# Kernel tuning notes

Measured on AMD Instinct MI355X. Metric: run time of the kernel, lower is better.

The kernel has to match this reference:

```python
import jax, jax.numpy as jnp
import numpy as np

NUM_STREAMS = 4
DIM = 256
SINKHORN_ITERS = 10
SINKHORN_TAU = 0.05


def sinkhorn_log(logits, num_iters=SINKHORN_ITERS, tau=SINKHORN_TAU):
    n = logits.shape[-1]
    z = logits / tau
    log_marginal = -jnp.log(jnp.asarray(float(n), dtype=logits.dtype))

    def body(carry, _):
        u, v = carry
        u = log_marginal - jax.scipy.special.logsumexp(z + v[None, :], axis=1)
        v = log_marginal - jax.scipy.special.logsumexp(z + u[:, None], axis=0)
        return (u, v), None

    u0 = jnp.zeros((n,), dtype=z.dtype)
    v0 = jnp.zeros((n,), dtype=z.dtype)
    (u, v), _ = jax.lax.scan(body, (u0, v0), None, length=num_iters)
    return jnp.exp(z + u[:, None] + v[None, :]) * n


def setup_inputs() -> dict:
    key = jax.random.key(0)
    k_res, k_w = jax.random.split(key)
    B = 65536
    residuals = jax.random.normal(k_res, (B, NUM_STREAMS, DIM), dtype=jnp.float32)
    # h_res_logits: -8 everywhere, 0 on diagonal (as in __init__)
    h_res_logits = jnp.full((NUM_STREAMS, NUM_STREAMS), -8.0, dtype=jnp.float32)
    h_res_logits = h_res_logits.at[jnp.arange(NUM_STREAMS), jnp.arange(NUM_STREAMS)].set(0.0)
    # h_pre_logits: -8 everywhere, 0 at init_residual_index=0
    h_pre_logits = jnp.full((NUM_STREAMS,), -8.0, dtype=jnp.float32).at[0].set(0.0)
    h_post_logits = jnp.zeros((NUM_STREAMS,), dtype=jnp.float32)
    # branch Linear(dim, dim, bias=False): weight (out, in), y = x @ W.T
    bound = 1.0 / np.sqrt(DIM)
    W_branch = jax.random.uniform(k_w, (DIM, DIM), dtype=jnp.float32, minval=-bound, maxval=bound)
    return {
        "residuals": residuals,
        "h_res_logits": h_res_logits,
        "h_pre_logits": h_pre_logits,
        "h_post_logits": h_post_logits,
        "W_branch": W_branch,
    }


def reference(residuals, h_res_logits, h_pre_logits, h_post_logits, W_branch):
    # residuals: (B, S, D)
    h_res = sinkhorn_log(h_res_logits)                     # (S, S) doubly-stochastic * n
    h_pre = jax.nn.softmax(h_pre_logits)                   # (S,)
    h_post = jax.nn.softmax(h_post_logits)                 # (S,)
    residuals_mixed = jnp.einsum('st,bsd->btd', h_res, residuals)
    branch_input = jnp.einsum('s,bsd->bd', h_pre, residuals)
    branch_output = branch_input @ W_branch.T              # (B, D)
    depth_out = jnp.einsum('bd,s->bsd', branch_output, h_post)
    return residuals_mixed + depth_out
```

## Files before the change

### kernel.cpp

```cpp
#include <hip/hip_runtime.h>

#define NSTREAMS 4
#define DIM 256
#define BM 16
#define NTHREADS 512
#define TILES 8

typedef __attribute__((ext_vector_type(8))) short short8;
typedef __attribute__((ext_vector_type(4))) float f32x4;

static __device__ __forceinline__ short f2bf(float x) {
    union { float f; unsigned int u; } c; c.f = x;
    unsigned int u = c.u;
    unsigned int lsb = (u >> 16) & 1u;
    u += 0x7fffu + lsb;
    return (short)(u >> 16);
}
static __device__ __forceinline__ float bf2f(short s) {
    union { unsigned int u; float f; } c;
    c.u = ((unsigned int)(unsigned short)s) << 16;
    return c.f;
}
static __device__ __forceinline__ int2 f2bf4(float4 v) {
    unsigned int lo, hi;
    asm("v_cvt_pk_bf16_f32 %0, %1, %2" : "=v"(lo) : "v"(v.x), "v"(v.y));
    asm("v_cvt_pk_bf16_f32 %0, %1, %2" : "=v"(hi) : "v"(v.z), "v"(v.w));
    int2 r; r.x = (int)lo; r.y = (int)hi;
    return r;
}
static __device__ __forceinline__ float4 bf4_2f(int2 p) {
    union { int2 v; short s[4]; } u; u.v = p;
    return make_float4(bf2f(u.s[0]), bf2f(u.s[1]), bf2f(u.s[2]), bf2f(u.s[3]));
}

static __device__ void compute_h(const float* __restrict__ hres_l,
                                 const float* __restrict__ hpre_l,
                                 const float* __restrict__ hpost_l,
                                 float* h_out) {
    const float inv_tau = 1.0f / 0.05f;
    float z[4][4];
    for (int i = 0; i < 4; ++i)
        for (int j = 0; j < 4; ++j)
            z[i][j] = hres_l[i * 4 + j] * inv_tau;
    float u[4] = {0.f, 0.f, 0.f, 0.f};
    float v[4] = {0.f, 0.f, 0.f, 0.f};
    const float logm = -logf(4.0f);
    for (int it = 0; it < 10; ++it) {
        for (int i = 0; i < 4; ++i) {
            float m = -1e30f;
            for (int j = 0; j < 4; ++j) m = fmaxf(m, z[i][j] + v[j]);
            float ss = 0.f;
            for (int j = 0; j < 4; ++j) ss += expf(z[i][j] + v[j] - m);
            u[i] = logm - (m + logf(ss));
        }
        for (int j = 0; j < 4; ++j) {
            float m = -1e30f;
            for (int i = 0; i < 4; ++i) m = fmaxf(m, z[i][j] + u[i]);
            float ss = 0.f;
            for (int i = 0; i < 4; ++i) ss += expf(z[i][j] + u[i] - m);
            v[j] = logm - (m + logf(ss));
        }
    }
    for (int i = 0; i < 4; ++i)
        for (int j = 0; j < 4; ++j)
            h_out[i * 4 + j] = expf(z[i][j] + u[i] + v[j]) * 4.0f;
    {
        float m = fmaxf(fmaxf(hpre_l[0], hpre_l[1]), fmaxf(hpre_l[2], hpre_l[3]));
        float e0 = expf(hpre_l[0] - m), e1 = expf(hpre_l[1] - m);
        float e2 = expf(hpre_l[2] - m), e3 = expf(hpre_l[3] - m);
        float ss = e0 + e1 + e2 + e3;
        h_out[16] = e0 / ss; h_out[17] = e1 / ss; h_out[18] = e2 / ss; h_out[19] = e3 / ss;
    }
    {
        float m = fmaxf(fmaxf(hpost_l[0], hpost_l[1]), fmaxf(hpost_l[2], hpost_l[3]));
        float e0 = expf(hpost_l[0] - m), e1 = expf(hpost_l[1] - m);
        float e2 = expf(hpost_l[2] - m), e3 = expf(hpost_l[3] - m);
        float ss = e0 + e1 + e2 + e3;
        h_out[20] = e0 / ss; h_out[21] = e1 / ss; h_out[22] = e2 / ss; h_out[23] = e3 / ss;
    }
}

__global__ void prep_h_kernel(const float* __restrict__ hres_l,
                              const float* __restrict__ hpre_l,
                              const float* __restrict__ hpost_l,
                              float* __restrict__ ws) {
    if (threadIdx.x == 0) compute_h(hres_l, hpre_l, hpost_l, ws);
}

__global__ __launch_bounds__(256) void prep_wh_kernel(const float* __restrict__ Wb,
                                                      short* __restrict__ wbf,
                                                      const float* __restrict__ hres_l,
                                                      const float* __restrict__ hpre_l,
                                                      const float* __restrict__ hpost_l,
                                                      float* __restrict__ ws_h) {
    int idx = blockIdx.x * 256 + threadIdx.x;
    float4 v = reinterpret_cast<const float4*>(Wb)[idx];
    reinterpret_cast<int2*>(wbf)[idx] = f2bf4(v);
    if (blockIdx.x == 0 && threadIdx.x == 0)
        compute_h(hres_l, hpre_l, hpost_l, ws_h);
}

template <bool USE_WSW>
__global__ __launch_bounds__(NTHREADS) void fused_kernel(
    const float* __restrict__ res,
    const float* __restrict__ Wb,
    const short* __restrict__ wbf,
    const float* __restrict__ hptr,
    const float* __restrict__ hres_l,
    const float* __restrict__ hpre_l,
    const float* __restrict__ hpost_l,
    float* __restrict__ out)
{
    __shared__ __align__(16) short res_lds[BM][NSTREAMS][DIM];
    __shared__ __align__(16) short bi_lds[BM][DIM + 8];
    __shared__ __align__(16) short bo_lds[BM][DIM + 8];
    __shared__ float h_sh[24];

    const int t  = threadIdx.x;
    const int d4 = t & 63;
    const int r0 = t >> 6;
    const int w  = t >> 6;
    const int l  = t & 63;
    const int lr = l & 15;
    const int lk = l >> 4;

    if (hptr) {
        if (t < 24) h_sh[t] = hptr[t];
    } else if (t == 0) {
        compute_h(hres_l, hpre_l, hpost_l, h_sh);
    }
    __syncthreads();

    const float hp0 = h_sh[16], hp1 = h_sh[17], hp2 = h_sh[18], hp3 = h_sh[19];
    float hres[4][4];
    #pragma unroll
    for (int s = 0; s < 4; ++s)
        #pragma unroll
        for (int tt = 0; tt < 4; ++tt)
            hres[s][tt] = h_sh[s * 4 + tt];
    float hq[4] = {h_sh[20], h_sh[21], h_sh[22], h_sh[23]};

    const long tile0 = (long)blockIdx.x * TILES;

    #pragma unroll
    for (int it = 0; it < 2; ++it) {
        int r = r0 + it * 8;
        const float4* p = reinterpret_cast<const float4*>(
            res + (tile0 * BM + r) * (NSTREAMS * DIM)) + d4;
        float4 v0 = p[0];
        float4 v1 = p[64];
        float4 v2 = p[128];
        float4 v3 = p[192];
        float4 bi;
        bi.x = hp0 * v0.x + hp1 * v1.x + hp2 * v2.x + hp3 * v3.x;
        bi.y = hp0 * v0.y + hp1 * v1.y + hp2 * v2.y + hp3 * v3.y;
        bi.z = hp0 * v0.z + hp1 * v1.z + hp2 * v2.z + hp3 * v3.z;
        bi.w = hp0 * v0.w + hp1 * v1.w + hp2 * v2.w + hp3 * v3.w;
        *reinterpret_cast<int2*>(&bi_lds[r][d4 * 4]) = f2bf4(bi);
        *reinterpret_cast<int2*>(&res_lds[r][0][d4 * 4]) = f2bf4(v0);
        *reinterpret_cast<int2*>(&res_lds[r][1][d4 * 4]) = f2bf4(v1);
        *reinterpret_cast<int2*>(&res_lds[r][2][d4 * 4]) = f2bf4(v2);
        *reinterpret_cast<int2*>(&res_lds[r][3][d4 * 4]) = f2bf4(v3);
    }
    __syncthreads();

    for (int ti = 0; ti < TILES; ++ti) {
        f32x4 acc[2] = {f32x4{0.f, 0.f, 0.f, 0.f}, f32x4{0.f, 0.f, 0.f, 0.f}};
        for (int k0 = 0; k0 < DIM; k0 += 32) {
            short8 a = *reinterpret_cast<const short8*>(&bi_lds[lr][k0 + lk * 8]);
            #pragma unroll
            for (int nt = 0; nt < 2; ++nt) {
                int dcol = w * 32 + nt * 16 + lr;
                short8 b;
                if (USE_WSW) {
                    b = *reinterpret_cast<const short8*>(wbf + dcol * DIM + k0 + lk * 8);
                } else {
                    const float4* wp = reinterpret_cast<const float4*>(Wb + dcol * DIM + k0 + lk * 8);
                    float4 wa = wp[0];
                    float4 wb2 = wp[1];
                    b[0] = f2bf(wa.x); b[1] = f2bf(wa.y); b[2] = f2bf(wa.z); b[3] = f2bf(wa.w);
                    b[4] = f2bf(wb2.x); b[5] = f2bf(wb2.y); b[6] = f2bf(wb2.z); b[7] = f2bf(wb2.w);
                }
                acc[nt] = __builtin_amdgcn_mfma_f32_16x16x32_bf16(a, b, acc[nt], 0, 0, 0);
            }
        }

        #pragma unroll
        for (int nt = 0; nt < 2; ++nt) {
            int d = w * 32 + nt * 16 + lr;
            #pragma unroll
            for (int j = 0; j < 4; ++j) {
                int m = lk * 4 + j;
                bo_lds[m][d] = f2bf(acc[nt][j]);
            }
        }

        int2 rsp[2][4];
        #pragma unroll
        for (int it = 0; it < 2; ++it) {
            int r = r0 + it * 8;
            #pragma unroll
            for (int s = 0; s < 4; ++s)
                rsp[it][s] = *reinterpret_cast<int2*>(&res_lds[r][s][d4 * 4]);
        }
        __syncthreads();

        float4 n[2][4];
        const bool more = (ti + 1 < TILES);
        if (more) {
            #pragma unroll
            for (int it = 0; it < 2; ++it) {
                int r = r0 + it * 8;
                const float4* p = reinterpret_cast<const float4*>(
                    res + ((tile0 + ti + 1) * BM + r) * (NSTREAMS * DIM)) + d4;
                n[it][0] = p[0];
                n[it][1] = p[64];
                n[it][2] = p[128];
                n[it][3] = p[192];
            }
        }

        #pragma unroll
        for (int it = 0; it < 2; ++it) {
            int r = r0 + it * 8;
            float4 bo  = bf4_2f(*reinterpret_cast<int2*>(&bo_lds[r][d4 * 4]));
            float4 rs0 = bf4_2f(rsp[it][0]);
            float4 rs1 = bf4_2f(rsp[it][1]);
            float4 rs2 = bf4_2f(rsp[it][2]);
            float4 rs3 = bf4_2f(rsp[it][3]);
            float* obase = out + (((tile0 + ti) * BM + r) * 4) * DIM + d4 * 4;
            #pragma unroll
            for (int tt = 0; tt < 4; ++tt) {
                float4 o;
                o.x = hq[tt] * bo.x + hres[0][tt] * rs0.x + hres[1][tt] * rs1.x + hres[2][tt] * rs2.x + hres[3][tt] * rs3.x;
                o.y = hq[tt] * bo.y + hres[0][tt] * rs0.y + hres[1][tt] * rs1.y + hres[2][tt] * rs2.y + hres[3][tt] * rs3.y;
                o.z = hq[tt] * bo.z + hres[0][tt] * rs0.z + hres[1][tt] * rs1.z + hres[2][tt] * rs2.z + hres[3][tt] * rs3.z;
                o.w = hq[tt] * bo.w + hres[0][tt] * rs0.w + hres[1][tt] * rs1.w + hres[2][tt] * rs2.w + hres[3][tt] * rs3.w;
                *reinterpret_cast<float4*>(obase + tt * DIM) = o;
            }
        }

        if (more) {
            #pragma unroll
            for (int it = 0; it < 2; ++it) {
                int r = r0 + it * 8;
                float4 bi;
                bi.x = hp0 * n[it][0].x + hp1 * n[it][1].x + hp2 * n[it][2].x + hp3 * n[it][3].x;
                bi.y = hp0 * n[it][0].y + hp1 * n[it][1].y + hp2 * n[it][2].y + hp3 * n[it][3].y;
                bi.z = hp0 * n[it][0].z + hp1 * n[it][1].z + hp2 * n[it][2].z + hp3 * n[it][3].z;
                bi.w = hp0 * n[it][0].w + hp1 * n[it][1].w + hp2 * n[it][2].w + hp3 * n[it][3].w;
                *reinterpret_cast<int2*>(&bi_lds[r][d4 * 4]) = f2bf4(bi);
                *reinterpret_cast<int2*>(&res_lds[r][0][d4 * 4]) = f2bf4(n[it][0]);
                *reinterpret_cast<int2*>(&res_lds[r][1][d4 * 4]) = f2bf4(n[it][1]);
                *reinterpret_cast<int2*>(&res_lds[r][2][d4 * 4]) = f2bf4(n[it][2]);
                *reinterpret_cast<int2*>(&res_lds[r][3][d4 * 4]) = f2bf4(n[it][3]);
            }
        }
        __syncthreads();
    }
}

extern "C" void kernel_launch(void* const* d_in, const int* in_sizes, int n_in,
                              void* d_out, int out_size, void* d_ws, size_t ws_size,
                              hipStream_t stream) {
    const float* res     = (const float*)d_in[0];
    const float* hres_l  = (const float*)d_in[1];
    const float* hpre_l  = (const float*)d_in[2];
    const float* hpost_l = (const float*)d_in[3];
    const float* Wb      = (const float*)d_in[4];
    float* out = (float*)d_out;

    const int Btot = in_sizes[0] / (NSTREAMS * DIM);
    const int grid = Btot / (BM * TILES);

    const size_t W_OFF = 256;
    const size_t need_h = 24 * sizeof(float);
    const size_t need_w = W_OFF + (size_t)DIM * DIM * sizeof(short);
    const bool has_h = ws_size >= need_h;
    const bool has_w = ws_size >= need_w;

    float* ws_h = (float*)d_ws;
    short* ws_w = (short*)((char*)d_ws + W_OFF);

    if (has_w) {
        prep_wh_kernel<<<(DIM * DIM / 4) / 256, 256, 0, stream>>>(
            Wb, ws_w, hres_l, hpre_l, hpost_l, ws_h);
        fused_kernel<true><<<grid, NTHREADS, 0, stream>>>(
            res, Wb, ws_w, ws_h, hres_l, hpre_l, hpost_l, out);
    } else if (has_h) {
        prep_h_kernel<<<1, 64, 0, stream>>>(hres_l, hpre_l, hpost_l, ws_h);
        fused_kernel<false><<<grid, NTHREADS, 0, stream>>>(
            res, Wb, nullptr, ws_h, hres_l, hpre_l, hpost_l, out);
    } else {
        fused_kernel<false><<<grid, NTHREADS, 0, stream>>>(
            res, Wb, nullptr, nullptr, hres_l, hpre_l, hpost_l, out);
    }
}
```

Measured before the change: 132.0 us.

## Keep residual tile in registers instead of LDS and store branch output as fp32

The residual tile is held in registers (cur/nx) instead of being staged as bf16 in LDS, so the per-tile LDS writes, reads and conversions for the residuals go away. The mixed residual term now uses full-precision inputs. The branch output is staged in LDS as fp32 instead of bf16, and __syncthreads is replaced by an explicit lgkmcnt wait plus s_barrier. The launch bounds now request a minimum occupancy of 4, which raises register pressure because of the extra float4 arrays and risks spills.

Measured after the change: 200.3 us. +51.7%, slower.

```diff
diff --git a/kernel.cpp b/kernel.cpp
--- a/kernel.cpp
+++ b/kernel.cpp
@@ -16,11 +16,6 @@
     u += 0x7fffu + lsb;
     return (short)(u >> 16);
 }
-static __device__ __forceinline__ float bf2f(short s) {
-    union { unsigned int u; float f; } c;
-    c.u = ((unsigned int)(unsigned short)s) << 16;
-    return c.f;
-}
 static __device__ __forceinline__ int2 f2bf4(float4 v) {
     unsigned int lo, hi;
     asm("v_cvt_pk_bf16_f32 %0, %1, %2" : "=v"(lo) : "v"(v.x), "v"(v.y));
@@ -28,9 +23,9 @@
     int2 r; r.x = (int)lo; r.y = (int)hi;
     return r;
 }
-static __device__ __forceinline__ float4 bf4_2f(int2 p) {
-    union { int2 v; short s[4]; } u; u.v = p;
-    return make_float4(bf2f(u.s[0]), bf2f(u.s[1]), bf2f(u.s[2]), bf2f(u.s[3]));
+
+static __device__ __forceinline__ void barrier_lgkm() {
+    asm volatile("s_waitcnt lgkmcnt(0)\n\ts_barrier" ::: "memory");
 }
 
 static __device__ void compute_h(const float* __restrict__ hres_l,
@@ -101,7 +96,7 @@
 }
 
 template <bool USE_WSW>
-__global__ __launch_bounds__(NTHREADS) void fused_kernel(
+__global__ __launch_bounds__(NTHREADS, 4) void fused_kernel(
     const float* __restrict__ res,
     const float* __restrict__ Wb,
     const short* __restrict__ wbf,
@@ -111,9 +106,8 @@
     const float* __restrict__ hpost_l,
     float* __restrict__ out)
 {
-    __shared__ __align__(16) short res_lds[BM][NSTREAMS][DIM];
     __shared__ __align__(16) short bi_lds[BM][DIM + 8];
-    __shared__ __align__(16) short bo_lds[BM][DIM + 8];
+    __shared__ __align__(16) float bo_lds[BM][DIM + 4];
     __shared__ float h_sh[24];
 
     const int t  = threadIdx.x;
@@ -129,7 +123,7 @@
     } else if (t == 0) {
         compute_h(hres_l, hpre_l, hpost_l, h_sh);
     }
-    __syncthreads();
+    barrier_lgkm();
 
     const float hp0 = h_sh[16], hp1 = h_sh[17], hp2 = h_sh[18], hp3 = h_sh[19];
     float hres[4][4];
@@ -142,27 +136,24 @@
 
     const long tile0 = (long)blockIdx.x * TILES;
 
+    float4 cur[2][4];
     #pragma unroll
     for (int it = 0; it < 2; ++it) {
         int r = r0 + it * 8;
         const float4* p = reinterpret_cast<const float4*>(
             res + (tile0 * BM + r) * (NSTREAMS * DIM)) + d4;
-        float4 v0 = p[0];
-        float4 v1 = p[64];
-        float4 v2 = p[128];
-        float4 v3 = p[192];
+        cur[it][0] = p[0];
+        cur[it][1] = p[64];
+        cur[it][2] = p[128];
+        cur[it][3] = p[192];
         float4 bi;
-        bi.x = hp0 * v0.x + hp1 * v1.x + hp2 * v2.x + hp3 * v3.x;
-        bi.y = hp0 * v0.y + hp1 * v1.y + hp2 * v2.y + hp3 * v3.y;
-        bi.z = hp0 * v0.z + hp1 * v1.z + hp2 * v2.z + hp3 * v3.z;
-        bi.w = hp0 * v0.w + hp1 * v1.w + hp2 * v2.w + hp3 * v3.w;
+        bi.x = hp0 * cur[it][0].x + hp1 * cur[it][1].x + hp2 * cur[it][2].x + hp3 * cur[it][3].x;
+        bi.y = hp0 * cur[it][0].y + hp1 * cur[it][1].y + hp2 * cur[it][2].y + hp3 * cur[it][3].y;
+        bi.z = hp0 * cur[it][0].z + hp1 * cur[it][1].z + hp2 * cur[it][2].z + hp3 * cur[it][3].z;
+        bi.w = hp0 * cur[it][0].w + hp1 * cur[it][1].w + hp2 * cur[it][2].w + hp3 * cur[it][3].w;
         *reinterpret_cast<int2*>(&bi_lds[r][d4 * 4]) = f2bf4(bi);
-        *reinterpret_cast<int2*>(&res_lds[r][0][d4 * 4]) = f2bf4(v0);
-        *reinterpret_cast<int2*>(&res_lds[r][1][d4 * 4]) = f2bf4(v1);
-        *reinterpret_cast<int2*>(&res_lds[r][2][d4 * 4]) = f2bf4(v2);
-        *reinterpret_cast<int2*>(&res_lds[r][3][d4 * 4]) = f2bf4(v3);
-    }
-    __syncthreads();
+    }
+    barrier_lgkm();
 
     for (int ti = 0; ti < TILES; ++ti) {
         f32x4 acc[2] = {f32x4{0.f, 0.f, 0.f, 0.f}, f32x4{0.f, 0.f, 0.f, 0.f}};
@@ -185,27 +176,7 @@
             }
         }
 
-        #pragma unroll
-        for (int nt = 0; nt < 2; ++nt) {
-            int d = w * 32 + nt * 16 + lr;
-            #pragma unroll
-            for (int j = 0; j < 4; ++j) {
-                int m = lk * 4 + j;
-                bo_lds[m][d] = f2bf(acc[nt][j]);
-            }
-        }
-
-        int2 rsp[2][4];
-        #pragma unroll
-        for (int it = 0; it < 2; ++it) {
-            int r = r0 + it * 8;
-            #pragma unroll
-            for (int s = 0; s < 4; ++s)
-                rsp[it][s] = *reinterpret_cast<int2*>(&res_lds[r][s][d4 * 4]);
-        }
-        __syncthreads();
-
-        float4 n[2][4];
+        float4 nx[2][4];
         const bool more = (ti + 1 < TILES);
         if (more) {
             #pragma unroll
@@ -213,29 +184,38 @@
                 int r = r0 + it * 8;
                 const float4* p = reinterpret_cast<const float4*>(
                     res + ((tile0 + ti + 1) * BM + r) * (NSTREAMS * DIM)) + d4;
-                n[it][0] = p[0];
-                n[it][1] = p[64];
-                n[it][2] = p[128];
-                n[it][3] = p[192];
-            }
-        }
+                nx[it][0] = p[0];
+                nx[it][1] = p[64];
+                nx[it][2] = p[128];
+                nx[it][3] = p[192];
+            }
+        }
+
+        #pragma unroll
+        for (int nt = 0; nt < 2; ++nt) {
+            int d = w * 32 + nt * 16 + lr;
+            #pragma unroll
+            for (int j = 0; j < 4; ++j)
+                bo_lds[lk * 4 + j][d] = acc[nt][j];
+        }
+        barrier_lgkm();
 
         #pragma unroll
         for (int it = 0; it < 2; ++it) {
             int r = r0 + it * 8;
-            float4 bo  = bf4_2f(*reinterpret_cast<int2*>(&bo_lds[r][d4 * 4]));
-            float4 rs0 = bf4_2f(rsp[it][0]);
-            float4 rs1 = bf4_2f(rsp[it][1]);
-            float4 rs2 = bf4_2f(rsp[it][2]);
-            float4 rs3 = bf4_2f(rsp[it][3]);
+            float4 bo = *reinterpret_cast<const float4*>(&bo_lds[r][d4 * 4]);
             float* obase = out + (((tile0 + ti) * BM + r) * 4) * DIM + d4 * 4;
             #pragma unroll
             for (int tt = 0; tt < 4; ++tt) {
                 float4 o;
-                o.x = hq[tt] * bo.x + hres[0][tt] * rs0.x + hres[1][tt] * rs1.x + hres[2][tt] * rs2.x + hres[3][tt] * rs3.x;
-                o.y = hq[tt] * bo.y + hres[0][tt] * rs0.y + hres[1][tt] * rs1.y + hres[2][tt] * rs2.y + hres[3][tt] * rs3.y;
-                o.z = hq[tt] * bo.z + hres[0][tt] * rs0.z + hres[1][tt] * rs1.z + hres[2][tt] * rs2.z + hres[3][tt] * rs3.z;
-                o.w = hq[tt] * bo.w + hres[0][tt] * rs0.w + hres[1][tt] * rs1.w + hres[2][tt] * rs2.w + hres[3][tt] * rs3.w;
+                o.x = hq[tt] * bo.x + hres[0][tt] * cur[it][0].x + hres[1][tt] * cur[it][1].x
+                    + hres[2][tt] * cur[it][2].x + hres[3][tt] * cur[it][3].x;
+                o.y = hq[tt] * bo.y + hres[0][tt] * cur[it][0].y + hres[1][tt] * cur[it][1].y
+                    + hres[2][tt] * cur[it][2].y + hres[3][tt] * cur[it][3].y;
+                o.z = hq[tt] * bo.z + hres[0][tt] * cur[it][0].z + hres[1][tt] * cur[it][1].z
+                    + hres[2][tt] * cur[it][2].z + hres[3][tt] * cur[it][3].z;
+                o.w = hq[tt] * bo.w + hres[0][tt] * cur[it][0].w + hres[1][tt] * cur[it][1].w
+                    + hres[2][tt] * cur[it][2].w + hres[3][tt] * cur[it][3].w;
                 *reinterpret_cast<float4*>(obase + tt * DIM) = o;
             }
         }
@@ -245,18 +225,17 @@
             for (int it = 0; it < 2; ++it) {
                 int r = r0 + it * 8;
                 float4 bi;
-                bi.x = hp0 * n[it][0].x + hp1 * n[it][1].x + hp2 * n[it][2].x + hp3 * n[it][3].x;
-                bi.y = hp0 * n[it][0].y + hp1 * n[it][1].y + hp2 * n[it][2].y + hp3 * n[it][3].y;
-                bi.z = hp0 * n[it][0].z + hp1 * n[it][1].z + hp2 * n[it][2].z + hp3 * n[it][3].z;
-                bi.w = hp0 * n[it][0].w + hp1 * n[it][1].w + hp2 * n[it][2].w + hp3 * n[it][3].w;
+                bi.x = hp0 * nx[it][0].x + hp1 * nx[it][1].x + hp2 * nx[it][2].x + hp3 * nx[it][3].x;
+                bi.y = hp0 * nx[it][0].y + hp1 * nx[it][1].y + hp2 * nx[it][2].y + hp3 * nx[it][3].y;
+                bi.z = hp0 * nx[it][0].z + hp1 * nx[it][1].z + hp2 * nx[it][2].z + hp3 * nx[it][3].z;
+                bi.w = hp0 * nx[it][0].w + hp1 * nx[it][1].w + hp2 * nx[it][2].w + hp3 * nx[it][3].w;
                 *reinterpret_cast<int2*>(&bi_lds[r][d4 * 4]) = f2bf4(bi);
-                *reinterpret_cast<int2*>(&res_lds[r][0][d4 * 4]) = f2bf4(n[it][0]);
-                *reinterpret_cast<int2*>(&res_lds[r][1][d4 * 4]) = f2bf4(n[it][1]);
-                *reinterpret_cast<int2*>(&res_lds[r][2][d4 * 4]) = f2bf4(n[it][2]);
-                *reinterpret_cast<int2*>(&res_lds[r][3][d4 * 4]) = f2bf4(n[it][3]);
-            }
-        }
-        __syncthreads();
+                #pragma unroll
+                for (int s = 0; s < 4; ++s)
+                    cur[it][s] = nx[it][s];
+            }
+        }
+        barrier_lgkm();
     }
 }
 
```
